# Kernel optimization log

Hardware: AMD Instinct MI355X
Metric: run time of the kernel (lower is better)

The kernel has to match this reference:

```python
import jax, jax.numpy as jnp
import numpy as np

N_USERS = 60000
N_ITEMS = 40000
N_NODES = N_USERS + N_ITEMS  # 100000
N_EDGES = 3_200_000
EMB_DIM = 64
N_LAYERS = 3
S_TEMP = 1.0  # config['s_temp']
EPS = 1e-16   # torch_geometric.utils.softmax denominator eps


def segment_softmax(logits, seg, num_segments):
    # numerically stable scatter-softmax (PyG softmax semantics)
    m = jax.ops.segment_max(logits, seg, num_segments=num_segments)
    m = jnp.where(jnp.isfinite(m), m, 0.0)  # empty segments -> -inf guard
    e = jnp.exp(logits - m[seg])
    s = jax.ops.segment_sum(e, seg, num_segments=num_segments)
    return e / (s[seg] + EPS)


def setup_inputs() -> dict:
    key = jax.random.key(0)
    k1, k2, k3 = jax.random.split(key, 3)
    # nn.Embedding weight, init normal(std=0.1) for non-NGCF models
    emb = jax.random.normal(k1, (N_NODES, EMB_DIM), dtype=jnp.float32) * 0.1
    edge_index = jax.random.randint(k2, (2, N_EDGES), 0, N_NODES, dtype=jnp.int32)
    edge_attrs = jax.random.normal(k3, (N_EDGES,), dtype=jnp.float32)
    return {"emb": emb, "edge_index": edge_index, "edge_attrs": edge_attrs}


def reference(emb, edge_index, edge_attrs):
    from_, to_ = edge_index[0], edge_index[1]
    logits = edge_attrs / S_TEMP
    incoming = segment_softmax(logits, to_, N_NODES)
    outgoing = segment_softmax(logits, from_, N_NODES)
    norm = jnp.sqrt(incoming * outgoing)  # abl_study == 0 branch

    embs = [emb]
    cur = emb
    for _ in range(N_LAYERS):
        # message: norm * x_j ; aggregate: scatter-add at to_
        msg = norm[:, None] * cur[from_]           # [E, D]
        cur = jax.ops.segment_sum(msg, to_, num_segments=N_NODES)  # [N, D]
        embs.append(cur)

    out = jnp.mean(jnp.stack(embs, axis=0), axis=0)  # lightGCN-style layer mean
    return (emb, out)
```

## Files before the change

### kernel.cpp

```cpp
#include <hip/hip_runtime.h>
#include <math.h>
#include <hip/hip_fp16.h>

#define N_NODES 100000
#define N_EDGES 3200000
#define EPS 1e-16f
#define BSH 8
#define BN 256
#define NBK 391
#define PTT 512
#define PE2 8
#define PTILE (PTT * PE2)
#define GR (PTILE / 16)
#define PBLOCKS ((N_EDGES + PTILE - 1) / PTILE)
#define CAP 9216u
#define FSPLIT 50000u
#define SCALE 8.0f

typedef float    f4v __attribute__((ext_vector_type(4)));
typedef float    f2v __attribute__((ext_vector_type(2)));

static __device__ __forceinline__ float4 nt_load_f4(const float4* p) {
    f4v v = __builtin_nontemporal_load((const f4v*)p);
    return make_float4(v.x, v.y, v.z, v.w);
}

static __device__ __forceinline__ unsigned short f_to_bf(float f) {
    unsigned u = __float_as_uint(f);
    unsigned r = (u + 0x7FFFu + ((u >> 16) & 1u)) >> 16;
    return (unsigned short)r;
}
static __device__ __forceinline__ float slot_w(unsigned s) {
    return __half2float(__ushort_as_half((unsigned short)(s >> 17)));
}
static __device__ __forceinline__ void fma8_fp8(float w, uint2 r, float* a) {
    f2v v0 = __builtin_amdgcn_cvt_pk_f32_fp8((int)r.x, false);
    f2v v1 = __builtin_amdgcn_cvt_pk_f32_fp8((int)r.x, true);
    f2v v2 = __builtin_amdgcn_cvt_pk_f32_fp8((int)r.y, false);
    f2v v3 = __builtin_amdgcn_cvt_pk_f32_fp8((int)r.y, true);
    a[0] = fmaf(w, v0.x, a[0]); a[1] = fmaf(w, v0.y, a[1]);
    a[2] = fmaf(w, v1.x, a[2]); a[3] = fmaf(w, v1.y, a[3]);
    a[4] = fmaf(w, v2.x, a[4]); a[5] = fmaf(w, v2.y, a[5]);
    a[6] = fmaf(w, v3.x, a[6]); a[7] = fmaf(w, v3.y, a[7]);
}
static __device__ __forceinline__ uint4 pack8(const float* a) {
    uint4 o;
    o.x = (unsigned)f_to_bf(a[0]) | ((unsigned)f_to_bf(a[1]) << 16);
    o.y = (unsigned)f_to_bf(a[2]) | ((unsigned)f_to_bf(a[3]) << 16);
    o.z = (unsigned)f_to_bf(a[4]) | ((unsigned)f_to_bf(a[5]) << 16);
    o.w = (unsigned)f_to_bf(a[6]) | ((unsigned)f_to_bf(a[7]) << 16);
    return o;
}
static __device__ __forceinline__ uint2 pack8_fp8(const float* a) {
    int w0 = __builtin_amdgcn_cvt_pk_fp8_f32(a[0], a[1], 0, false);
    w0 = __builtin_amdgcn_cvt_pk_fp8_f32(a[2], a[3], w0, true);
    int w1 = __builtin_amdgcn_cvt_pk_fp8_f32(a[4], a[5], 0, false);
    w1 = __builtin_amdgcn_cvt_pk_fp8_f32(a[6], a[7], w1, true);
    return make_uint2((unsigned)w0, (unsigned)w1);
}
static __device__ __forceinline__ float bfu_to_f(unsigned u, int hi) {
    return __uint_as_float(hi ? (u & 0xFFFF0000u) : (u << 16));
}

__global__ __launch_bounds__(PTT) void partition(
        const int* __restrict__ ei, const float* __restrict__ attr,
        unsigned* __restrict__ pos_t, unsigned* __restrict__ pos_f,
        uint2* __restrict__ bt, unsigned* __restrict__ bf) {
    __shared__ unsigned ht[NBK], hf[NBK];
    __shared__ unsigned hbt[NBK + 1], hbf[NBK + 1];
    __shared__ unsigned dlt[NBK], dlf[NBK];
    __shared__ unsigned short lutT[GR], lutF[GR];
    __shared__ unsigned wsum[8];
    __shared__ unsigned sbtx[PTILE], sbty[PTILE];
    __shared__ unsigned sbf[PTILE];
    const int tid = threadIdx.x;
    const int lane = tid & 63, wid = tid >> 6;
    for (int i = tid; i < NBK; i += PTT) { ht[i] = 0; hf[i] = 0; }
    __syncthreads();
    const int tile = blockIdx.x * PTILE;
    const int tcount = (tile + PTILE < N_EDGES) ? PTILE : (N_EDGES - tile);
    unsigned fv[PE2], tv[PE2];
    float xv[PE2];
    #pragma unroll
    for (int k = 0; k < PE2; ++k) {
        int e = tile + k * PTT + tid;
        if (e < N_EDGES) {
            fv[k] = (unsigned)__builtin_nontemporal_load(&ei[e]);
            tv[k] = (unsigned)__builtin_nontemporal_load(&ei[N_EDGES + e]);
            xv[k] = __expf(__builtin_nontemporal_load(&attr[e]));
            atomicAdd(&ht[tv[k] >> BSH], 1u);
            atomicAdd(&hf[fv[k] >> BSH], 1u);
        } else {
            tv[k] = 0xFFFFFFFFu;
        }
    }
    __syncthreads();
    unsigned ot = (tid < NBK) ? ht[tid] : 0u;
    unsigned of = (tid < NBK) ? hf[tid] : 0u;
    unsigned own = ot | (of << 16);
    unsigned x = own;
    #pragma unroll
    for (int d = 1; d < 64; d <<= 1) {
        unsigned v = __shfl_up(x, d, 64);
        if (lane >= d) x += v;
    }
    if (lane == 63) wsum[wid] = x;
    __syncthreads();
    unsigned pre = 0;
    for (int w = 0; w < wid; ++w) pre += wsum[w];
    unsigned excl = x + pre - own;
    unsigned et = excl & 0xFFFFu, ef = excl >> 16;
    if (tid < NBK) {
        hbt[tid] = et;
        hbf[tid] = ef;
        unsigned rt = ot ? atomicAdd(&pos_t[tid], ot) : 0u;
        unsigned rf = of ? atomicAdd(&pos_f[tid], of) : 0u;
        dlt[tid] = tid * CAP + rt - et;
        dlf[tid] = tid * CAP + rf - ef;
    }
    if (tid == NBK - 1) { hbt[NBK] = et + ot; hbf[NBK] = ef + of; }
    __syncthreads();
    if (tid < NBK) {
        unsigned b0 = hbt[tid], b1 = hbt[tid + 1];
        for (unsigned g = (b0 + 15u) >> 4; (g << 4) < b1; ++g) lutT[g] = (unsigned short)tid;
        b0 = hbf[tid]; b1 = hbf[tid + 1];
        for (unsigned g = (b0 + 15u) >> 4; (g << 4) < b1; ++g) lutF[g] = (unsigned short)tid;
    }
    for (int i = tid; i < NBK; i += PTT) { ht[i] = hbt[i]; hf[i] = hbf[i]; }
    __syncthreads();
    #pragma unroll
    for (int k = 0; k < PE2; ++k) {
        if (tv[k] != 0xFFFFFFFFu) {
            unsigned p = atomicAdd(&ht[tv[k] >> BSH], 1u);
            sbtx[p] = fv[k] | ((tv[k] & (BN - 1u)) << 17);
            sbty[p] = __float_as_uint(xv[k]);
            unsigned q = atomicAdd(&hf[fv[k] >> BSH], 1u);
            sbf[q] = ((fv[k] & (BN - 1u)) << 16) |
                     (unsigned)__half_as_ushort(__float2half(xv[k]));
        }
    }
    __syncthreads();
    for (int i = tid; i < tcount; i += PTT) {
        unsigned b = lutT[i >> 4];
        while (hbt[b + 1] <= (unsigned)i) ++b;
        unsigned ga = dlt[b] + (unsigned)i;
        if (ga < (b + 1u) * CAP) bt[ga] = make_uint2(sbtx[i], sbty[i]);
    }
    for (int i = tid; i < tcount; i += PTT) {
        unsigned b = lutF[i >> 4];
        while (hbf[b + 1] <= (unsigned)i) ++b;
        unsigned ga = dlf[b] + (unsigned)i;
        if (ga < (b + 1u) * CAP) bf[ga] = sbf[i];
    }
}

__global__ __launch_bounds__(1024) void bucket_sum_f(
        const unsigned* __restrict__ pos_f, const unsigned* __restrict__ bf,
        float* __restrict__ s_from_inv,
        const float4* __restrict__ emb4, uint2* __restrict__ emb_f8) {
    __shared__ float s[BN];
    int b = blockIdx.x, tid = threadIdx.x;
    if (tid < BN) s[tid] = 0.f;
    __syncthreads();
    unsigned fill = pos_f[b]; if (fill > CAP) fill = CAP;
    unsigned lo = b * CAP, hi = lo + fill;
    for (unsigned i = lo + tid; i < hi; i += 1024) {
        unsigned u = __builtin_nontemporal_load(&bf[i]);
        atomicAdd(&s[u >> 16], __half2float(__ushort_as_half((unsigned short)(u & 0xFFFFu))));
    }
    __syncthreads();
    if (tid < BN) {
        int node = b * BN + tid;
        if (node < N_NODES) s_from_inv[node] = rsqrtf(s[tid] + EPS);
    }
    int nl = tid >> 2;
    int part = tid & 3;
    int node = b * BN + nl;
    if (node < N_NODES) {
        float rsv = rsqrtf(s[nl] + EPS) * SCALE;
        size_t rbase = (size_t)node * 16 + part * 4;
        #pragma unroll
        for (int c = 0; c < 2; ++c) {
            float4 v0 = emb4[rbase + c * 2];
            float4 v1 = emb4[rbase + c * 2 + 1];
            float a[8] = {v0.x * rsv, v0.y * rsv, v0.z * rsv, v0.w * rsv,
                          v1.x * rsv, v1.y * rsv, v1.z * rsv, v1.w * rsv};
            emb_f8[(size_t)node * 8 + part * 2 + c] = pack8_fp8(a);
        }
    }
}

__global__ __launch_bounds__(1024) void bucket_csr_t(
        const unsigned* __restrict__ pos_t, const uint2* __restrict__ bt,
        const float* __restrict__ s_from_inv,
        uint2* __restrict__ row2, unsigned* __restrict__ slots,
        float2* __restrict__ sc2) {
    __shared__ unsigned cntL[BN], cntH[BN];
    __shared__ float sto[BN];
    __shared__ unsigned curL[BN], curH[BN];
    __shared__ unsigned wsum[16];
    int b = blockIdx.x, tid = threadIdx.x;
    const int lane = tid & 63, wid = tid >> 6;
    if (tid < BN) { cntL[tid] = 0; cntH[tid] = 0; sto[tid] = 0.f; }
    __syncthreads();
    unsigned fill = pos_t[b]; if (fill > CAP) fill = CAP;
    unsigned lo = b * CAP, hi = lo + fill;
    for (unsigned i = lo + tid; i < hi; i += 1024) {
        uint2 u = bt[i];
        unsigned tl = u.x >> 17;
        unsigned f = u.x & 0x1FFFFu;
        atomicAdd((f < FSPLIT) ? &cntL[tl] : &cntH[tl], 1u);
        atomicAdd(&sto[tl], __uint_as_float(u.y));
    }
    __syncthreads();
    unsigned ol = (tid < BN) ? cntL[tid] : 0u;
    unsigned oh = (tid < BN) ? cntH[tid] : 0u;
    unsigned own = ol + oh;
    unsigned x = own;
    #pragma unroll
    for (int d = 1; d < 64; d <<= 1) {
        unsigned v = __shfl_up(x, d, 64);
        if (lane >= d) x += v;
    }
    if (lane == 63) wsum[wid] = x;
    __syncthreads();
    unsigned pre = 0;
    for (int w = 0; w < wid; ++w) pre += wsum[w];
    unsigned excl = x + pre - own;
    if (tid < BN) {
        int node = b * BN + tid;
        if (node < N_NODES) {
            row2[node] = make_uint2(lo + excl, lo + excl + own);
            float rt = rsqrtf(sto[tid] + EPS);
            sc2[node] = make_float2(rt * (1.0f / SCALE), rt * s_from_inv[node]);
        }
        curL[tid] = lo + excl;
        curH[tid] = lo + excl + ol;
    }
    __syncthreads();
    for (unsigned i = lo + tid; i < hi; i += 1024) {
        uint2 u = bt[i];
        unsigned tl = u.x >> 17;
        unsigned f = u.x & 0x1FFFFu;
        unsigned hb = (unsigned)__half_as_ushort(__float2half(__uint_as_float(u.y)));
        unsigned p = atomicAdd((f < FSPLIT) ? &curL[tl] : &curH[tl], 1u);
        slots[p] = f | (hb << 17);
    }
}

#define GATHER_CORE8(TABLE)                                                       \
    float a[8] = {0, 0, 0, 0, 0, 0, 0, 0};                                        \
    float bacc[8] = {0, 0, 0, 0, 0, 0, 0, 0};                                     \
    unsigned k = beg;                                                             \
    for (; k + 8 <= end; k += 8) {                                                \
        unsigned s0 = slots[k], s1 = slots[k + 1], s2 = slots[k + 2], s3 = slots[k + 3]; \
        unsigned s4 = slots[k + 4], s5 = slots[k + 5], s6 = slots[k + 6], s7 = slots[k + 7]; \
        uint2 r0 = TABLE[(size_t)(s0 & 0x1FFFFu) * 8 + lane];                     \
        uint2 r1 = TABLE[(size_t)(s1 & 0x1FFFFu) * 8 + lane];                     \
        uint2 r2 = TABLE[(size_t)(s2 & 0x1FFFFu) * 8 + lane];                     \
        uint2 r3 = TABLE[(size_t)(s3 & 0x1FFFFu) * 8 + lane];                     \
        uint2 r4 = TABLE[(size_t)(s4 & 0x1FFFFu) * 8 + lane];                     \
        uint2 r5 = TABLE[(size_t)(s5 & 0x1FFFFu) * 8 + lane];                     \
        uint2 r6 = TABLE[(size_t)(s6 & 0x1FFFFu) * 8 + lane];                     \
        uint2 r7 = TABLE[(size_t)(s7 & 0x1FFFFu) * 8 + lane];                     \
        fma8_fp8(slot_w(s0), r0, a);    fma8_fp8(slot_w(s1), r1, bacc);           \
        fma8_fp8(slot_w(s2), r2, a);    fma8_fp8(slot_w(s3), r3, bacc);           \
        fma8_fp8(slot_w(s4), r4, a);    fma8_fp8(slot_w(s5), r5, bacc);           \
        fma8_fp8(slot_w(s6), r6, a);    fma8_fp8(slot_w(s7), r7, bacc);           \
    }                                                                             \
    for (; k < end; ++k) {                                                        \
        unsigned s = slots[k];                                                    \
        uint2 r = TABLE[(size_t)(s & 0x1FFFFu) * 8 + lane];                       \
        fma8_fp8(slot_w(s), r, a);                                                \
    }                                                                             \
    _Pragma("unroll")                                                             \
    for (int j = 0; j < 8; ++j) a[j] += bacc[j];

__global__ void prop1(const uint2* __restrict__ row2, const unsigned* __restrict__ slots,
                      const uint2* __restrict__ emb_f8, const float2* __restrict__ sc2,
                      uint2* __restrict__ T1f8, uint4* __restrict__ T1bf,
                      const float4* __restrict__ emb4, float4* __restrict__ out_emb4) {
    int node = blockIdx.x * 32 + (threadIdx.x >> 3);
    int lane = threadIdx.x & 7;
    if (node < N_NODES) {
        uint2 rp = row2[node];
        unsigned beg = rp.x, end = rp.y;
        GATHER_CORE8(emb_f8)
        float2 sc = sc2[node];
        float own[8], tab[8];
        #pragma unroll
        for (int j = 0; j < 8; ++j) { own[j] = a[j] * sc.x; tab[j] = a[j] * sc.y; }
        size_t o = (size_t)node * 8 + lane;
        T1bf[o] = pack8(own);
        T1f8[o] = pack8_fp8(tab);
    }
    const int total = N_NODES * 16;
    const int stride = ((N_NODES * 8 + 255) / 256) * 256;
    for (int i = blockIdx.x * 256 + threadIdx.x; i < total; i += stride) {
        out_emb4[i] = nt_load_f4(&emb4[i]);
    }
}

__global__ void prop2(const uint2* __restrict__ row2, const unsigned* __restrict__ slots,
                      const uint2* __restrict__ T1f8, const float2* __restrict__ sc2,
                      uint2* __restrict__ T2f8, uint4* __restrict__ T2bf) {
    int node = blockIdx.x * 32 + (threadIdx.x >> 3);
    int lane = threadIdx.x & 7;
    if (node >= N_NODES) return;
    uint2 rp = row2[node];
    unsigned beg = rp.x, end = rp.y;
    GATHER_CORE8(T1f8)
    float2 sc = sc2[node];
    float own[8], tab[8];
    #pragma unroll
    for (int j = 0; j < 8; ++j) { own[j] = a[j] * sc.x; tab[j] = a[j] * sc.y; }
    size_t o = (size_t)node * 8 + lane;
    T2bf[o] = pack8(own);
    T2f8[o] = pack8_fp8(tab);
}

__global__ void prop3(const uint2* __restrict__ row2, const unsigned* __restrict__ slots,
                      const uint2* __restrict__ T2f8, const float2* __restrict__ sc2,
                      const uint4* __restrict__ T1bf, const uint4* __restrict__ T2bf,
                      const float4* __restrict__ emb4, float4* __restrict__ acc) {
    int node = blockIdx.x * 32 + (threadIdx.x >> 3);
    int lane = threadIdx.x & 7;
    if (node >= N_NODES) return;
    uint2 rp = row2[node];
    unsigned beg = rp.x, end = rp.y;
    GATHER_CORE8(T2f8)
    float osc = sc2[node].x;
    size_t o = (size_t)node * 8 + lane;
    uint4 t1 = T1bf[o];
    uint4 t2 = T2bf[o];
    unsigned tw1[4] = {t1.x, t1.y, t1.z, t1.w};
    unsigned tw2[4] = {t2.x, t2.y, t2.z, t2.w};
    size_t o4 = (size_t)node * 16 + lane * 2;
    float4 e0 = emb4[o4], e1 = emb4[o4 + 1];
    float e[8] = {e0.x, e0.y, e0.z, e0.w, e1.x, e1.y, e1.z, e1.w};
    float r[8];
    #pragma unroll
    for (int j = 0; j < 8; ++j) {
        float l1v = bfu_to_f(tw1[j >> 1], j & 1);
        float l2v = bfu_to_f(tw2[j >> 1], j & 1);
        r[j] = (e[j] + l1v + l2v + a[j] * osc) * 0.25f;
    }
    acc[o4]     = make_float4(r[0], r[1], r[2], r[3]);
    acc[o4 + 1] = make_float4(r[4], r[5], r[6], r[7]);
}

extern "C" void kernel_launch(void* const* d_in, const int* in_sizes, int n_in,
                              void* d_out, int out_size, void* d_ws, size_t ws_size,
                              hipStream_t stream) {
    const float* emb = (const float*)d_in[0];
    const int* ei = (const int*)d_in[1];
    const float* attr = (const float*)d_in[2];

    float* out_emb = (float*)d_out;
    float* out_acc = out_emb + (size_t)N_NODES * 64;

    char* ws = (char*)d_ws;
    size_t off = 0;
    auto alloc = [&](size_t bytes) -> void* {
        void* p = ws + off;
        off += (bytes + 255) & ~(size_t)255;
        return p;
    };
    unsigned* pos_t   = (unsigned*)alloc((size_t)NBK * 4);
    unsigned* pos_f   = (unsigned*)alloc((size_t)NBK * 4);
    size_t zero_bytes = off;
    uint2*    row2    = (uint2*)   alloc((size_t)N_NODES * 8);
    float* s_from_inv = (float*)   alloc((size_t)N_NODES * 4);
    float2*   sc2     = (float2*)  alloc((size_t)N_NODES * 8);
    uint2* bt         = (uint2*)   alloc((size_t)NBK * CAP * 8);
    unsigned* bfa     = (unsigned*)alloc((size_t)NBK * CAP * 4);
    unsigned* slots   = bfa;
    uint2* emb_f8     = (uint2*)   alloc((size_t)N_NODES * 64);
    uint2* T1f8       = (uint2*)   alloc((size_t)N_NODES * 64);
    uint4* T1bf       = (uint4*)   alloc((size_t)N_NODES * 128);
    uint2* T2f8 = (uint2*)bt;
    uint4* T2bf = (uint4*)((char*)bt + (size_t)N_NODES * 64);
    (void)ws_size;

    hipMemsetAsync(d_ws, 0, zero_bytes, stream);

    partition<<<PBLOCKS, PTT, 0, stream>>>(ei, attr, pos_t, pos_f, bt, bfa);
    bucket_sum_f<<<NBK, 1024, 0, stream>>>(pos_f, bfa, s_from_inv,
                                           (const float4*)emb, emb_f8);
    bucket_csr_t<<<NBK, 1024, 0, stream>>>(pos_t, bt, s_from_inv, row2, slots, sc2);

    const int pgrid = (N_NODES * 8 + 255) / 256;
    prop1<<<pgrid, 256, 0, stream>>>(row2, slots, emb_f8, sc2, T1f8, T1bf,
                                     (const float4*)emb, (float4*)out_emb);
    prop2<<<pgrid, 256, 0, stream>>>(row2, slots, T1f8, sc2, T2f8, T2bf);
    prop3<<<pgrid, 256, 0, stream>>>(row2, slots, T2f8, sc2, T1bf, T2bf,
                                     (const float4*)emb, (float4*)out_acc);
}
```

Measured before the change: 252.4 us.

## Fuse bucket sum and CSR kernels, sort slots into four source ranges

Merges the from-side softmax sum kernel and the to-side CSR build kernel into one kernel per bucket. The per-node rsqrt of the from-sum now stays in shared memory instead of going through a global s_from_inv array, which also saves one kernel launch. Edges within each destination row are now grouped by four source-index ranges instead of two, aiming to improve cache locality of the embedding gathers in the propagation kernels. The cost is more shared-memory counters and atomics per node, and a longer fused kernel that may have lower occupancy.

```diff
diff --git a/kernel.cpp b/kernel.cpp
--- a/kernel.cpp
+++ b/kernel.cpp
@@ -14,7 +14,7 @@
 #define GR (PTILE / 16)
 #define PBLOCKS ((N_EDGES + PTILE - 1) / PTILE)
 #define CAP 9216u
-#define FSPLIT 50000u
+#define NR 4
 #define SCALE 8.0f
 
 typedef float    f4v __attribute__((ext_vector_type(4)));
@@ -23,6 +23,9 @@
 static __device__ __forceinline__ float4 nt_load_f4(const float4* p) {
     f4v v = __builtin_nontemporal_load((const f4v*)p);
     return make_float4(v.x, v.y, v.z, v.w);
+}
+static __device__ __forceinline__ int range_of(unsigned f) {
+    return (f >= 50000u) ? (f >= 75000u ? 3 : 2) : (f >= 25000u ? 1 : 0);
 }
 
 static __device__ __forceinline__ unsigned short f_to_bf(float f) {
@@ -154,88 +157,88 @@
     }
 }
 
-__global__ __launch_bounds__(1024) void bucket_sum_f(
+__global__ __launch_bounds__(1024) void bucket_build(
         const unsigned* __restrict__ pos_f, const unsigned* __restrict__ bf,
-        float* __restrict__ s_from_inv,
-        const float4* __restrict__ emb4, uint2* __restrict__ emb_f8) {
-    __shared__ float s[BN];
-    int b = blockIdx.x, tid = threadIdx.x;
-    if (tid < BN) s[tid] = 0.f;
-    __syncthreads();
-    unsigned fill = pos_f[b]; if (fill > CAP) fill = CAP;
-    unsigned lo = b * CAP, hi = lo + fill;
-    for (unsigned i = lo + tid; i < hi; i += 1024) {
-        unsigned u = __builtin_nontemporal_load(&bf[i]);
-        atomicAdd(&s[u >> 16], __half2float(__ushort_as_half((unsigned short)(u & 0xFFFFu))));
-    }
-    __syncthreads();
-    if (tid < BN) {
-        int node = b * BN + tid;
-        if (node < N_NODES) s_from_inv[node] = rsqrtf(s[tid] + EPS);
-    }
-    int nl = tid >> 2;
-    int part = tid & 3;
-    int node = b * BN + nl;
-    if (node < N_NODES) {
-        float rsv = rsqrtf(s[nl] + EPS) * SCALE;
-        size_t rbase = (size_t)node * 16 + part * 4;
-        #pragma unroll
-        for (int c = 0; c < 2; ++c) {
-            float4 v0 = emb4[rbase + c * 2];
-            float4 v1 = emb4[rbase + c * 2 + 1];
-            float a[8] = {v0.x * rsv, v0.y * rsv, v0.z * rsv, v0.w * rsv,
-                          v1.x * rsv, v1.y * rsv, v1.z * rsv, v1.w * rsv};
-            emb_f8[(size_t)node * 8 + part * 2 + c] = pack8_fp8(a);
-        }
-    }
-}
-
-__global__ __launch_bounds__(1024) void bucket_csr_t(
         const unsigned* __restrict__ pos_t, const uint2* __restrict__ bt,
-        const float* __restrict__ s_from_inv,
+        const float4* __restrict__ emb4, uint2* __restrict__ emb_f8,
         uint2* __restrict__ row2, unsigned* __restrict__ slots,
         float2* __restrict__ sc2) {
-    __shared__ unsigned cntL[BN], cntH[BN];
+    __shared__ float s[BN];
     __shared__ float sto[BN];
-    __shared__ unsigned curL[BN], curH[BN];
-    __shared__ unsigned wsum[16];
+    __shared__ unsigned cnt[BN][NR];
+    __shared__ unsigned cur[BN][NR];
+    __shared__ unsigned wsum[4];
     int b = blockIdx.x, tid = threadIdx.x;
     const int lane = tid & 63, wid = tid >> 6;
-    if (tid < BN) { cntL[tid] = 0; cntH[tid] = 0; sto[tid] = 0.f; }
-    __syncthreads();
+    if (tid < BN) {
+        s[tid] = 0.f;
+        sto[tid] = 0.f;
+        #pragma unroll
+        for (int r = 0; r < NR; ++r) cnt[tid][r] = 0;
+    }
+    __syncthreads();
+    {
+        unsigned fill = pos_f[b]; if (fill > CAP) fill = CAP;
+        unsigned lo = b * CAP, hi = lo + fill;
+        for (unsigned i = lo + tid; i < hi; i += 1024) {
+            unsigned u = __builtin_nontemporal_load(&bf[i]);
+            atomicAdd(&s[u >> 16], __half2float(__ushort_as_half((unsigned short)(u & 0xFFFFu))));
+        }
+    }
+    __syncthreads();
+    {
+        int nl = tid >> 2, part = tid & 3;
+        int node = b * BN + nl;
+        if (node < N_NODES) {
+            float rsv = rsqrtf(s[nl] + EPS) * SCALE;
+            size_t rbase = (size_t)node * 16 + part * 4;
+            #pragma unroll
+            for (int c = 0; c < 2; ++c) {
+                float4 v0 = emb4[rbase + c * 2];
+                float4 v1 = emb4[rbase + c * 2 + 1];
+                float a[8] = {v0.x * rsv, v0.y * rsv, v0.z * rsv, v0.w * rsv,
+                              v1.x * rsv, v1.y * rsv, v1.z * rsv, v1.w * rsv};
+                emb_f8[(size_t)node * 8 + part * 2 + c] = pack8_fp8(a);
+            }
+        }
+    }
     unsigned fill = pos_t[b]; if (fill > CAP) fill = CAP;
     unsigned lo = b * CAP, hi = lo + fill;
     for (unsigned i = lo + tid; i < hi; i += 1024) {
         uint2 u = bt[i];
         unsigned tl = u.x >> 17;
         unsigned f = u.x & 0x1FFFFu;
-        atomicAdd((f < FSPLIT) ? &cntL[tl] : &cntH[tl], 1u);
+        atomicAdd(&cnt[tl][range_of(f)], 1u);
         atomicAdd(&sto[tl], __uint_as_float(u.y));
     }
     __syncthreads();
-    unsigned ol = (tid < BN) ? cntL[tid] : 0u;
-    unsigned oh = (tid < BN) ? cntH[tid] : 0u;
-    unsigned own = ol + oh;
+    unsigned c0 = 0, c1 = 0, c2 = 0, c3 = 0, own = 0;
+    if (tid < BN) {
+        c0 = cnt[tid][0]; c1 = cnt[tid][1]; c2 = cnt[tid][2]; c3 = cnt[tid][3];
+        own = c0 + c1 + c2 + c3;
+    }
     unsigned x = own;
     #pragma unroll
     for (int d = 1; d < 64; d <<= 1) {
         unsigned v = __shfl_up(x, d, 64);
         if (lane >= d) x += v;
     }
-    if (lane == 63) wsum[wid] = x;
-    __syncthreads();
-    unsigned pre = 0;
-    for (int w = 0; w < wid; ++w) pre += wsum[w];
-    unsigned excl = x + pre - own;
+    if (tid < BN && lane == 63) wsum[wid] = x;
+    __syncthreads();
     if (tid < BN) {
+        unsigned pre = 0;
+        for (int w = 0; w < wid; ++w) pre += wsum[w];
+        unsigned base = lo + x + pre - own;
         int node = b * BN + tid;
         if (node < N_NODES) {
-            row2[node] = make_uint2(lo + excl, lo + excl + own);
+            row2[node] = make_uint2(base, base + own);
             float rt = rsqrtf(sto[tid] + EPS);
-            sc2[node] = make_float2(rt * (1.0f / SCALE), rt * s_from_inv[node]);
+            sc2[node] = make_float2(rt * (1.0f / SCALE), rt * rsqrtf(s[tid] + EPS));
         }
-        curL[tid] = lo + excl;
-        curH[tid] = lo + excl + ol;
+        cur[tid][0] = base;
+        cur[tid][1] = base + c0;
+        cur[tid][2] = base + c0 + c1;
+        cur[tid][3] = base + c0 + c1 + c2;
     }
     __syncthreads();
     for (unsigned i = lo + tid; i < hi; i += 1024) {
@@ -243,7 +246,7 @@
         unsigned tl = u.x >> 17;
         unsigned f = u.x & 0x1FFFFu;
         unsigned hb = (unsigned)__half_as_ushort(__float2half(__uint_as_float(u.y)));
-        unsigned p = atomicAdd((f < FSPLIT) ? &curL[tl] : &curH[tl], 1u);
+        unsigned p = atomicAdd(&cur[tl][range_of(f)], 1u);
         slots[p] = f | (hb << 17);
     }
 }
@@ -370,7 +373,6 @@
     unsigned* pos_f   = (unsigned*)alloc((size_t)NBK * 4);
     size_t zero_bytes = off;
     uint2*    row2    = (uint2*)   alloc((size_t)N_NODES * 8);
-    float* s_from_inv = (float*)   alloc((size_t)N_NODES * 4);
     float2*   sc2     = (float2*)  alloc((size_t)N_NODES * 8);
     uint2* bt         = (uint2*)   alloc((size_t)NBK * CAP * 8);
     unsigned* bfa     = (unsigned*)alloc((size_t)NBK * CAP * 4);
@@ -385,9 +387,9 @@
     hipMemsetAsync(d_ws, 0, zero_bytes, stream);
 
     partition<<<PBLOCKS, PTT, 0, stream>>>(ei, attr, pos_t, pos_f, bt, bfa);
-    bucket_sum_f<<<NBK, 1024, 0, stream>>>(pos_f, bfa, s_from_inv,
-                                           (const float4*)emb, emb_f8);
-    bucket_csr_t<<<NBK, 1024, 0, stream>>>(pos_t, bt, s_from_inv, row2, slots, sc2);
+    bucket_build<<<NBK, 1024, 0, stream>>>(pos_f, bfa, pos_t, bt,
+                                           (const float4*)emb, emb_f8,
+                                           row2, slots, sc2);
 
     const int pgrid = (N_NODES * 8 + 255) / 256;
     prop1<<<pgrid, 256, 0, stream>>>(row2, slots, emb_f8, sc2, T1f8, T1bf,
```

Measured after the change: 244.8 us. -3.0%, faster.
